# Kernel optimization log

Hardware: AMD Instinct MI355X
Metric: run time of the kernel (lower is better)

The kernel has to match this reference:

```python
import jax, jax.numpy as jnp
import numpy as np

B, T, C, UNITS = 64, 1000, 320, 320


def _lstm_scan(x_tbc, m_tb, W, U, b):
    """Masked LSTM over leading time axis.
    x_tbc: [T,B,C], m_tb: [T,B] bool. Keras gate order i,f,c(g),o.
    Masked steps carry (h,c) through unchanged and emit the carried h,
    matching Keras masking semantics. Returns (ys [T,B,U], h_T [B,U]).
    """
    units = U.shape[0]
    h0 = jnp.zeros((x_tbc.shape[1], units), x_tbc.dtype)

    def step(carry, inp):
        h, c = carry
        xt, mt = inp
        z = xt @ W + h @ U + b                      # [B, 4U]
        i, f, g, o = jnp.split(z, 4, axis=-1)
        i = jax.nn.sigmoid(i)
        f = jax.nn.sigmoid(f)
        g = jnp.tanh(g)
        o = jax.nn.sigmoid(o)
        c_new = f * c + i * g
        h_new = o * jnp.tanh(c_new)
        mt = mt[:, None]
        h = jnp.where(mt, h_new, h)
        c = jnp.where(mt, c_new, c)
        return (h, c), h

    (hT, cT), ys = jax.lax.scan(step, (h0, h0), (x_tbc, m_tb))
    return ys, hT


def setup_inputs() -> dict:
    key = jax.random.key(0)
    ks = jax.random.split(key, 8)
    inputs = jax.random.normal(ks[0], (B, T, C), dtype=jnp.float32)
    # padding mask: variable sequence lengths in [T//2, T]
    seq_len = jax.random.randint(ks[1], (B,), T // 2, T + 1)
    mask = (jnp.arange(T)[None, :] < seq_len[:, None])  # [B, T] bool
    s_in = 1.0 / np.sqrt(C)
    s_rec = 1.0 / np.sqrt(UNITS)
    W_fwd = jax.random.normal(ks[2], (C, 4 * UNITS), jnp.float32) * s_in
    U_fwd = jax.random.normal(ks[3], (UNITS, 4 * UNITS), jnp.float32) * s_rec
    b_fwd = jnp.zeros((4 * UNITS,), jnp.float32).at[UNITS:2 * UNITS].set(1.0)  # unit forget bias
    W_bwd = jax.random.normal(ks[4], (C, 4 * UNITS), jnp.float32) * s_in
    U_bwd = jax.random.normal(ks[5], (UNITS, 4 * UNITS), jnp.float32) * s_rec
    b_bwd = jnp.zeros((4 * UNITS,), jnp.float32).at[UNITS:2 * UNITS].set(1.0)
    return {"inputs": inputs, "mask": mask, "W_fwd": W_fwd, "U_fwd": U_fwd,
            "b_fwd": b_fwd, "W_bwd": W_bwd, "U_bwd": U_bwd, "b_bwd": b_bwd}


def reference(inputs, mask, W_fwd, U_fwd, b_fwd, W_bwd, U_bwd, b_bwd):
    x = jnp.transpose(inputs, (1, 0, 2))   # [T,B,C]
    m = jnp.transpose(mask, (1, 0))        # [T,B]
    # forward direction
    ys_f, h_f = _lstm_scan(x, m, W_fwd, U_fwd, b_fwd)
    # backward direction: go_backwards reverses time; Bidirectional flips output back
    ys_b, h_b = _lstm_scan(x[::-1], m[::-1], W_bwd, U_bwd, b_bwd)
    ys_b = ys_b[::-1]
    sequence_output = jnp.transpose(jnp.concatenate([ys_f, ys_b], axis=-1), (1, 0, 2))  # [B,T,2U]
    state_output = jnp.concatenate([h_f, h_b], axis=-1)  # [B,2U]
    return sequence_output, state_output
```

## Files before the change

### kernel.cpp

```cpp
#include <hip/hip_runtime.h>
#include <hip/hip_bf16.h>
#include <stdint.h>


#define Bx 64
#define Tx 1000
#define Cx 320
#define NSLICE 40
#define UPW 8

typedef __attribute__((ext_vector_type(8))) short short8;
typedef __attribute__((ext_vector_type(4))) short short4v;
typedef __attribute__((ext_vector_type(4))) float f32x4;

__device__ inline unsigned short f2bf(float f) {
  unsigned x = __builtin_bit_cast(unsigned, f);
  x += 0x7fffu + ((x >> 16) & 1u);
  return (unsigned short)(x >> 16);
}
__device__ inline float bf2f(unsigned short u) {
  unsigned x = ((unsigned)u) << 16;
  return __builtin_bit_cast(float, x);
}

#define OFF_MB   0ull
#define OFF_BAR  8192ull
#define OFF_HB   16384ull
#define OFF_XB   0ull
#define OFF_WT   40960000ull
#define OFF_BP   42598400ull
#define OFF_ZX   42608640ull

__global__ __launch_bounds__(256) void k_prep_x(const float* __restrict__ X,
                                                unsigned short* __restrict__ Xb) {
  int i4 = blockIdx.x * 256 + threadIdx.x;
  if (i4 >= Bx * Tx * Cx / 4) return;
  int idx = i4 * 4;
  int b = idx / (Tx * Cx);
  int rem = idx - b * (Tx * Cx);
  int t = rem / Cx;
  int c = rem - t * Cx;
  float4 v = *(const float4*)(X + idx);
  short4v o;
  o[0] = (short)f2bf(v.x); o[1] = (short)f2bf(v.y);
  o[2] = (short)f2bf(v.z); o[3] = (short)f2bf(v.w);
  *(short4v*)(Xb + (size_t)(t * Bx + b) * Cx + c) = o;
}

__global__ __launch_bounds__(256) void k_prep_w(const float* __restrict__ Wf,
                                                const float* __restrict__ Wb,
                                                const float* __restrict__ bfv,
                                                const float* __restrict__ bbv,
                                                unsigned short* __restrict__ Wt,
                                                float* __restrict__ biasp) {
  int gid = blockIdx.x * 256 + threadIdx.x;
  if (gid < 2 * 1280 * 320) {
    int dir = gid / (1280 * 320);
    int rem = gid - dir * 1280 * 320;
    int n = rem / 320;
    int k = rem - n * 320;
    int u = n >> 2, g = n & 3;
    const float* W = dir ? Wb : Wf;
    Wt[gid] = f2bf(W[k * 1280 + g * 320 + u]);
  }
  if (gid < 2 * 1280) {
    int dir = gid / 1280, n = gid - dir * 1280;
    int u = n >> 2, g = n & 3;
    const float* bsrc = dir ? bbv : bfv;
    biasp[gid] = bsrc[g * 320 + u];
  }
}

__global__ __launch_bounds__(256) void k_prep_mask(const void* __restrict__ maskp,
                                                   unsigned long long* __restrict__ mask2) {
  int t = blockIdx.x * 256 + threadIdx.x;
  if (t >= Tx) return;
  const unsigned* mw = (const unsigned*)maskp;
  const bool mbyte = (mw[0] == 0x01010101u);
  unsigned long long wv = 0ull;
  if (mbyte) {
    const unsigned char* m8 = (const unsigned char*)maskp;
#pragma unroll 8
    for (int b = 0; b < Bx; b++)
      wv |= (unsigned long long)(m8[b * Tx + t] & 1) << b;
  } else {
    const int* m32 = (const int*)maskp;
#pragma unroll 8
    for (int b = 0; b < Bx; b++)
      wv |= (unsigned long long)(m32[b * Tx + t] & 1) << b;
  }
  mask2[t] = wv;
}

__global__ __launch_bounds__(256) void k_gemm(const unsigned short* __restrict__ A,
                                              const unsigned short* __restrict__ Bt,
                                              const float* __restrict__ biasp,
                                              unsigned short* __restrict__ Czx) {
  int bid = blockIdx.x;
  int dir = bid / 5000;
  int r = bid - dir * 5000;
  int tm = r / 10, tn = r - (r / 10) * 10;
  long m0 = (long)tm * 128;
  int n0 = tn * 128;
  const unsigned short* Bd = Bt + (size_t)dir * 1280 * 320;
  const float* bias = biasp + dir * 1280;

  __shared__ __align__(16) unsigned short As[128 * 64];
  __shared__ __align__(16) unsigned short Bs[128 * 64];

  int tid = threadIdx.x;
  int wave = tid >> 6, lane = tid & 63;
  int l15 = lane & 15, l4 = lane >> 4;

  f32x4 acc[2][8];
#pragma unroll
  for (int i = 0; i < 2; i++)
#pragma unroll
    for (int j = 0; j < 8; j++) acc[i][j] = (f32x4){0.f, 0.f, 0.f, 0.f};

  for (int k0 = 0; k0 < 320; k0 += 64) {
    __syncthreads();
#pragma unroll
    for (int it = 0; it < 4; it++) {
      int idx = it * 256 + tid;
      int rr = idx >> 3, cc = idx & 7;
      const unsigned short* ga = A + (size_t)(m0 + rr) * 320 + k0 + cc * 8;
      unsigned short* la = As + (size_t)(it * 256 + wave * 64) * 8;
      __builtin_amdgcn_global_load_lds(
          (const __attribute__((address_space(1))) void*)ga,
          (__attribute__((address_space(3))) void*)la, 16, 0, 0);
      const unsigned short* gb = Bd + (size_t)(n0 + rr) * 320 + k0 + cc * 8;
      unsigned short* lb = Bs + (size_t)(it * 256 + wave * 64) * 8;
      __builtin_amdgcn_global_load_lds(
          (const __attribute__((address_space(1))) void*)gb,
          (__attribute__((address_space(3))) void*)lb, 16, 0, 0);
    }
    __syncthreads();
#pragma unroll
    for (int kk = 0; kk < 2; kk++) {
      short8 af[2], bf8[8];
#pragma unroll
      for (int mf = 0; mf < 2; mf++)
        af[mf] = *(const short8*)(As + (wave * 32 + mf * 16 + l15) * 64 + kk * 32 + l4 * 8);
#pragma unroll
      for (int nf = 0; nf < 8; nf++)
        bf8[nf] = *(const short8*)(Bs + (nf * 16 + l15) * 64 + kk * 32 + l4 * 8);
#pragma unroll
      for (int mf = 0; mf < 2; mf++)
#pragma unroll
        for (int nf = 0; nf < 8; nf++)
          acc[mf][nf] = __builtin_amdgcn_mfma_f32_16x16x32_bf16(af[mf], bf8[nf], acc[mf][nf], 0, 0, 0);
    }
  }
#pragma unroll
  for (int mf = 0; mf < 2; mf++) {
#pragma unroll
    for (int nf = 0; nf < 8; nf++) {
      int col = n0 + nf * 16 + l15;
      float bv = bias[col];
      int slice = col >> 5, i32v = col & 31;
      size_t sbase = ((size_t)(dir * NSLICE + slice)) * Tx * 2048;
#pragma unroll
      for (int i = 0; i < 4; i++) {
        long m = m0 + wave * 32 + mf * 16 + l4 * 4 + i;
        long t = m >> 6;
        int b = (int)(m & 63);
        Czx[sbase + (size_t)t * 2048 + b * 32 + i32v] = f2bf(acc[mf][nf][i] + bv);
      }
    }
  }
}

__global__ __launch_bounds__(256, 1) void k_lstm(const unsigned short* __restrict__ Zx,
                                                 const float* __restrict__ Uf,
                                                 const float* __restrict__ Ub,
                                                 const unsigned long long* __restrict__ mask2,
                                                 unsigned short* __restrict__ hbuf,
                                                 float* __restrict__ out,
                                                 unsigned* __restrict__ bar) {
  const int w = blockIdx.x;
  const int dir = w / NSLICE;
  const int slice = w - dir * NSLICE;
  const int u0 = slice * UPW;
  const int tid = threadIdx.x;
  const int wave = tid >> 6, lane = tid & 63;
  const int l15 = lane & 15, l4 = lane >> 4;

  const float* U = dir ? Ub : Uf;
  short8 bfrag[2][10];
#pragma unroll
  for (int nf = 0; nf < 2; nf++) {
    int i32v = nf * 16 + l15;
    int colU = (i32v & 3) * 320 + u0 + (i32v >> 2);
#pragma unroll
    for (int kt = 0; kt < 10; kt++) {
      short8 v;
#pragma unroll
      for (int j = 0; j < 8; j++)
        v[j] = (short)f2bf(U[(size_t)(kt * 32 + l4 * 8 + j) * 1280 + colU]);
      bfrag[nf][kt] = v;
    }
  }

  const int pb = tid >> 2;
  const int uu2 = (tid & 3) * 2;
  const int arow = wave * 16 + l15;
  float c0 = 0.f, c1 = 0.f, h0 = 0.f, h1 = 0.f;

  __shared__ float zsh[64][32];

  unsigned* slots = bar + (size_t)dir * NSLICE * 16;
  const unsigned short* zbase = Zx + ((size_t)(dir * NSLICE + slice)) * Tx * 2048;

  int t = dir ? (Tx - 1) : 0;
  short8 zv = *(const short8*)(zbase + (size_t)t * 2048 + tid * 8);
  unsigned long long mwrd = mask2[t];

  for (int s = 0;; ++s) {
    t = dir ? (Tx - 1 - s) : s;
    float zr[8];
    if (s > 0) {
      if (tid < NSLICE) {
        while (__hip_atomic_load(&slots[tid * 16], __ATOMIC_RELAXED,
                                 __HIP_MEMORY_SCOPE_AGENT) < (unsigned)s)
          __builtin_amdgcn_s_sleep(1);
      }
      __syncthreads();

      const unsigned short* hr = hbuf + ((size_t)((s & 1) * 2 + dir)) * Bx * 320;
      const unsigned short* hp = hr + arow * 320 + l4 * 8;
      short8 afr[10];
#pragma unroll
      for (int kt = 0; kt < 10; kt++) {
        union { unsigned long long q[2]; short8 v; } u;
        u.q[0] = __hip_atomic_load((const unsigned long long*)(hp + kt * 32),
                                   __ATOMIC_RELAXED, __HIP_MEMORY_SCOPE_AGENT);
        u.q[1] = __hip_atomic_load((const unsigned long long*)(hp + kt * 32 + 4),
                                   __ATOMIC_RELAXED, __HIP_MEMORY_SCOPE_AGENT);
        afr[kt] = u.v;
      }
#pragma unroll
      for (int nf = 0; nf < 2; nf++) {
        f32x4 a0 = {0.f, 0.f, 0.f, 0.f}, a1 = {0.f, 0.f, 0.f, 0.f};
#pragma unroll
        for (int k2 = 0; k2 < 5; k2++) {
          a0 = __builtin_amdgcn_mfma_f32_16x16x32_bf16(afr[2 * k2], bfrag[nf][2 * k2], a0, 0, 0, 0);
          a1 = __builtin_amdgcn_mfma_f32_16x16x32_bf16(afr[2 * k2 + 1], bfrag[nf][2 * k2 + 1], a1, 0, 0, 0);
        }
        int rr = wave * 16 + l4 * 4;
        zsh[rr + 0][nf * 16 + l15] = a0[0] + a1[0];
        zsh[rr + 1][nf * 16 + l15] = a0[1] + a1[1];
        zsh[rr + 2][nf * 16 + l15] = a0[2] + a1[2];
        zsh[rr + 3][nf * 16 + l15] = a0[3] + a1[3];
      }
      __syncthreads();
#pragma unroll
      for (int j = 0; j < 8; j++) zr[j] = zsh[pb][uu2 * 4 + j];
    } else {
#pragma unroll
      for (int j = 0; j < 8; j++) zr[j] = 0.f;
    }

    int mv = (int)((mwrd >> pb) & 1ull);
    {
      float zi = bf2f((unsigned short)zv[0]) + zr[0];
      float zf = bf2f((unsigned short)zv[1]) + zr[1];
      float zg = bf2f((unsigned short)zv[2]) + zr[2];
      float zo = bf2f((unsigned short)zv[3]) + zr[3];
      float ig = 1.f / (1.f + __expf(-zi));
      float fg = 1.f / (1.f + __expf(-zf));
      float gg = 2.f / (1.f + __expf(-2.f * zg)) - 1.f;
      float og = 1.f / (1.f + __expf(-zo));
      float cn = fg * c0 + ig * gg;
      float hn = og * (2.f / (1.f + __expf(-2.f * cn)) - 1.f);
      if (mv) { c0 = cn; h0 = hn; }
    }
    {
      float zi = bf2f((unsigned short)zv[4]) + zr[4];
      float zf = bf2f((unsigned short)zv[5]) + zr[5];
      float zg = bf2f((unsigned short)zv[6]) + zr[6];
      float zo = bf2f((unsigned short)zv[7]) + zr[7];
      float ig = 1.f / (1.f + __expf(-zi));
      float fg = 1.f / (1.f + __expf(-zf));
      float gg = 2.f / (1.f + __expf(-2.f * zg)) - 1.f;
      float og = 1.f / (1.f + __expf(-zo));
      float cn = fg * c1 + ig * gg;
      float hn = og * (2.f / (1.f + __expf(-2.f * cn)) - 1.f);
      if (mv) { c1 = cn; h1 = hn; }
    }

    unsigned short* hw = hbuf + ((size_t)(((s + 1) & 1) * 2 + dir)) * Bx * 320;
    unsigned hv = (unsigned)f2bf(h0) | ((unsigned)f2bf(h1) << 16);
    __hip_atomic_store((unsigned*)(hw + pb * 320 + u0 + uu2), hv,
                       __ATOMIC_RELAXED, __HIP_MEMORY_SCOPE_AGENT);

    __syncthreads();
    if (tid == 0 && s < Tx - 1)
      __hip_atomic_store(&slots[slice * 16], (unsigned)(s + 1), __ATOMIC_RELEASE,
                         __HIP_MEMORY_SCOPE_AGENT);

    *(float2*)(out + ((size_t)pb * Tx + t) * 640 + dir * 320 + u0 + uu2) =
        make_float2(h0, h1);
    if (s == Tx - 1) {
      *(float2*)(out + 40960000ull + (size_t)pb * 640 + dir * 320 + u0 + uu2) =
          make_float2(h0, h1);
      break;
    }

    int tn = dir ? (Tx - 2 - s) : (s + 1);
    zv = *(const short8*)(zbase + (size_t)tn * 2048 + tid * 8);
    mwrd = mask2[tn];
  }
}

extern "C" void kernel_launch(void* const* d_in, const int* in_sizes, int n_in,
                              void* d_out, int out_size, void* d_ws, size_t ws_size,
                              hipStream_t stream) {
  const float* X = (const float*)d_in[0];
  const void* Mk = d_in[1];
  const float* Wf = (const float*)d_in[2];
  const float* Uf = (const float*)d_in[3];
  const float* bfv = (const float*)d_in[4];
  const float* Wb = (const float*)d_in[5];
  const float* Ub = (const float*)d_in[6];
  const float* bbv = (const float*)d_in[7];

  char* ws = (char*)d_ws;
  unsigned short* Xb = (unsigned short*)(ws + OFF_XB);
  unsigned short* Wt = (unsigned short*)(ws + OFF_WT);
  float* bp = (float*)(ws + OFF_BP);
  unsigned short* Zx = (unsigned short*)(ws + OFF_ZX);
  unsigned long long* mask2 = (unsigned long long*)(ws + OFF_MB);
  unsigned short* hbuf = (unsigned short*)(ws + OFF_HB);
  unsigned* bar = (unsigned*)(ws + OFF_BAR);

  k_prep_x<<<dim3(20000), dim3(256), 0, stream>>>(X, Xb);
  k_prep_w<<<dim3(3200), dim3(256), 0, stream>>>(Wf, Wb, bfv, bbv, Wt, bp);
  k_gemm<<<dim3(10000), dim3(256), 0, stream>>>(Xb, Wt, bp, Zx);
  hipMemsetAsync(ws + OFF_BAR, 0, 5120, stream);
  k_prep_mask<<<dim3(4), dim3(256), 0, stream>>>(Mk, mask2);
  k_lstm<<<dim3(2 * NSLICE), dim3(256), 0, stream>>>(Zx, Uf, Ub, mask2, hbuf,
                                                     (float*)d_out, bar);
}
```

Baseline: 6.358 ms.

## Halve LSTM workgroups per direction, doubling units per workgroup

Changes the persistent recurrent kernel split from 40 to 20 workgroups per direction, so each handles 16 hidden units (64 gate columns), with a matching Zx layout in the GEMM epilogue. Each step now polls half as many cross-workgroup flags, which reduces grid-barrier traffic on the serial critical path. In exchange, each workgroup does twice the MFMA and gate math per step and holds twice the U fragments in registers. Output and h stores are widened to 64-bit, and the output writes switch to relaxed atomic stores.

```diff
diff --git a/kernel.cpp b/kernel.cpp
--- a/kernel.cpp
+++ b/kernel.cpp
@@ -6,8 +6,8 @@
 #define Bx 64
 #define Tx 1000
 #define Cx 320
-#define NSLICE 40
-#define UPW 8
+#define NSLICE 20
+#define UPW 16
 
 typedef __attribute__((ext_vector_type(8))) short short8;
 typedef __attribute__((ext_vector_type(4))) short short4v;
@@ -158,14 +158,14 @@
     for (int nf = 0; nf < 8; nf++) {
       int col = n0 + nf * 16 + l15;
       float bv = bias[col];
-      int slice = col >> 5, i32v = col & 31;
-      size_t sbase = ((size_t)(dir * NSLICE + slice)) * Tx * 2048;
+      int slice = col >> 6, i64v = col & 63;
+      size_t sbase = ((size_t)(dir * NSLICE + slice)) * Tx * 4096;
 #pragma unroll
       for (int i = 0; i < 4; i++) {
         long m = m0 + wave * 32 + mf * 16 + l4 * 4 + i;
         long t = m >> 6;
         int b = (int)(m & 63);
-        Czx[sbase + (size_t)t * 2048 + b * 32 + i32v] = f2bf(acc[mf][nf][i] + bv);
+        Czx[sbase + (size_t)t * 4096 + b * 64 + i64v] = f2bf(acc[mf][nf][i] + bv);
       }
     }
   }
@@ -187,11 +187,11 @@
   const int l15 = lane & 15, l4 = lane >> 4;
 
   const float* U = dir ? Ub : Uf;
-  short8 bfrag[2][10];
-#pragma unroll
-  for (int nf = 0; nf < 2; nf++) {
-    int i32v = nf * 16 + l15;
-    int colU = (i32v & 3) * 320 + u0 + (i32v >> 2);
+  short8 bfrag[4][10];
+#pragma unroll
+  for (int nf = 0; nf < 4; nf++) {
+    int ncol = nf * 16 + l15;
+    int colU = (ncol & 3) * 320 + u0 + (ncol >> 2);
 #pragma unroll
     for (int kt = 0; kt < 10; kt++) {
       short8 v;
@@ -203,22 +203,24 @@
   }
 
   const int pb = tid >> 2;
-  const int uu2 = (tid & 3) * 2;
+  const int uq = tid & 3;
   const int arow = wave * 16 + l15;
-  float c0 = 0.f, c1 = 0.f, h0 = 0.f, h1 = 0.f;
-
-  __shared__ float zsh[64][32];
-
-  unsigned* slots = bar + (size_t)dir * NSLICE * 16;
-  const unsigned short* zbase = Zx + ((size_t)(dir * NSLICE + slice)) * Tx * 2048;
+  float c0 = 0.f, c1 = 0.f, c2 = 0.f, c3 = 0.f;
+  float h0 = 0.f, h1 = 0.f, h2 = 0.f, h3 = 0.f;
+
+  __shared__ float zsh[64][68];
+
+  unsigned* slots = bar + dir * NSLICE * 16;
+  const unsigned short* zbase = Zx + ((size_t)(dir * NSLICE + slice)) * Tx * 4096;
 
   int t = dir ? (Tx - 1) : 0;
-  short8 zv = *(const short8*)(zbase + (size_t)t * 2048 + tid * 8);
+  short8 zv0 = *(const short8*)(zbase + (size_t)t * 4096 + pb * 64 + uq * 16);
+  short8 zv1 = *(const short8*)(zbase + (size_t)t * 4096 + pb * 64 + uq * 16 + 8);
   unsigned long long mwrd = mask2[t];
 
   for (int s = 0;; ++s) {
     t = dir ? (Tx - 1 - s) : s;
-    float zr[8];
+    float4 zr0, zr1, zr2, zr3;
     if (s > 0) {
       if (tid < NSLICE) {
         while (__hip_atomic_load(&slots[tid * 16], __ATOMIC_RELAXED,
@@ -240,7 +242,7 @@
         afr[kt] = u.v;
       }
 #pragma unroll
-      for (int nf = 0; nf < 2; nf++) {
+      for (int nf = 0; nf < 4; nf++) {
         f32x4 a0 = {0.f, 0.f, 0.f, 0.f}, a1 = {0.f, 0.f, 0.f, 0.f};
 #pragma unroll
         for (int k2 = 0; k2 < 5; k2++) {
@@ -254,44 +256,40 @@
         zsh[rr + 3][nf * 16 + l15] = a0[3] + a1[3];
       }
       __syncthreads();
-#pragma unroll
-      for (int j = 0; j < 8; j++) zr[j] = zsh[pb][uu2 * 4 + j];
+      zr0 = *(const float4*)&zsh[pb][uq * 16 + 0];
+      zr1 = *(const float4*)&zsh[pb][uq * 16 + 4];
+      zr2 = *(const float4*)&zsh[pb][uq * 16 + 8];
+      zr3 = *(const float4*)&zsh[pb][uq * 16 + 12];
     } else {
-#pragma unroll
-      for (int j = 0; j < 8; j++) zr[j] = 0.f;
+      zr0 = zr1 = zr2 = zr3 = make_float4(0.f, 0.f, 0.f, 0.f);
     }
 
     int mv = (int)((mwrd >> pb) & 1ull);
-    {
-      float zi = bf2f((unsigned short)zv[0]) + zr[0];
-      float zf = bf2f((unsigned short)zv[1]) + zr[1];
-      float zg = bf2f((unsigned short)zv[2]) + zr[2];
-      float zo = bf2f((unsigned short)zv[3]) + zr[3];
-      float ig = 1.f / (1.f + __expf(-zi));
-      float fg = 1.f / (1.f + __expf(-zf));
-      float gg = 2.f / (1.f + __expf(-2.f * zg)) - 1.f;
-      float og = 1.f / (1.f + __expf(-zo));
-      float cn = fg * c0 + ig * gg;
-      float hn = og * (2.f / (1.f + __expf(-2.f * cn)) - 1.f);
-      if (mv) { c0 = cn; h0 = hn; }
-    }
-    {
-      float zi = bf2f((unsigned short)zv[4]) + zr[4];
-      float zf = bf2f((unsigned short)zv[5]) + zr[5];
-      float zg = bf2f((unsigned short)zv[6]) + zr[6];
-      float zo = bf2f((unsigned short)zv[7]) + zr[7];
-      float ig = 1.f / (1.f + __expf(-zi));
-      float fg = 1.f / (1.f + __expf(-zf));
-      float gg = 2.f / (1.f + __expf(-2.f * zg)) - 1.f;
-      float og = 1.f / (1.f + __expf(-zo));
-      float cn = fg * c1 + ig * gg;
-      float hn = og * (2.f / (1.f + __expf(-2.f * cn)) - 1.f);
-      if (mv) { c1 = cn; h1 = hn; }
-    }
+#define GATES(CC, HH, Z0, Z1, Z2, Z3, ZR)                              \
+    {                                                                  \
+      float zi = bf2f((unsigned short)(Z0)) + (ZR).x;                  \
+      float zf = bf2f((unsigned short)(Z1)) + (ZR).y;                  \
+      float zg = bf2f((unsigned short)(Z2)) + (ZR).z;                  \
+      float zo = bf2f((unsigned short)(Z3)) + (ZR).w;                  \
+      float ig = 1.f / (1.f + __expf(-zi));                            \
+      float fg = 1.f / (1.f + __expf(-zf));                            \
+      float gg = 2.f / (1.f + __expf(-2.f * zg)) - 1.f;                \
+      float og = 1.f / (1.f + __expf(-zo));                            \
+      float cn = fg * (CC) + ig * gg;                                  \
+      float hn = og * (2.f / (1.f + __expf(-2.f * cn)) - 1.f);         \
+      if (mv) { (CC) = cn; (HH) = hn; }                                \
+    }
+    GATES(c0, h0, zv0[0], zv0[1], zv0[2], zv0[3], zr0)
+    GATES(c1, h1, zv0[4], zv0[5], zv0[6], zv0[7], zr1)
+    GATES(c2, h2, zv1[0], zv1[1], zv1[2], zv1[3], zr2)
+    GATES(c3, h3, zv1[4], zv1[5], zv1[6], zv1[7], zr3)
+#undef GATES
 
     unsigned short* hw = hbuf + ((size_t)(((s + 1) & 1) * 2 + dir)) * Bx * 320;
-    unsigned hv = (unsigned)f2bf(h0) | ((unsigned)f2bf(h1) << 16);
-    __hip_atomic_store((unsigned*)(hw + pb * 320 + u0 + uu2), hv,
+    unsigned long long hv =
+        (unsigned long long)f2bf(h0) | ((unsigned long long)f2bf(h1) << 16) |
+        ((unsigned long long)f2bf(h2) << 32) | ((unsigned long long)f2bf(h3) << 48);
+    __hip_atomic_store((unsigned long long*)(hw + pb * 320 + u0 + uq * 4), hv,
                        __ATOMIC_RELAXED, __HIP_MEMORY_SCOPE_AGENT);
 
     __syncthreads();
@@ -299,16 +297,23 @@
       __hip_atomic_store(&slots[slice * 16], (unsigned)(s + 1), __ATOMIC_RELEASE,
                          __HIP_MEMORY_SCOPE_AGENT);
 
-    *(float2*)(out + ((size_t)pb * Tx + t) * 640 + dir * 320 + u0 + uu2) =
-        make_float2(h0, h1);
+    union { float f[4]; unsigned long long q[2]; } ou;
+    ou.f[0] = h0; ou.f[1] = h1; ou.f[2] = h2; ou.f[3] = h3;
+    unsigned long long* op = (unsigned long long*)(out +
+        ((size_t)pb * Tx + t) * 640 + dir * 320 + u0 + uq * 4);
+    __hip_atomic_store(op, ou.q[0], __ATOMIC_RELAXED, __HIP_MEMORY_SCOPE_AGENT);
+    __hip_atomic_store(op + 1, ou.q[1], __ATOMIC_RELAXED, __HIP_MEMORY_SCOPE_AGENT);
     if (s == Tx - 1) {
-      *(float2*)(out + 40960000ull + (size_t)pb * 640 + dir * 320 + u0 + uu2) =
-          make_float2(h0, h1);
+      unsigned long long* fp = (unsigned long long*)(out + 40960000ull +
+          (size_t)pb * 640 + dir * 320 + u0 + uq * 4);
+      __hip_atomic_store(fp, ou.q[0], __ATOMIC_RELAXED, __HIP_MEMORY_SCOPE_AGENT);
+      __hip_atomic_store(fp + 1, ou.q[1], __ATOMIC_RELAXED, __HIP_MEMORY_SCOPE_AGENT);
       break;
     }
 
     int tn = dir ? (Tx - 2 - s) : (s + 1);
-    zv = *(const short8*)(zbase + (size_t)tn * 2048 + tid * 8);
+    zv0 = *(const short8*)(zbase + (size_t)tn * 4096 + pb * 64 + uq * 16);
+    zv1 = *(const short8*)(zbase + (size_t)tn * 4096 + pb * 64 + uq * 16 + 8);
     mwrd = mask2[tn];
   }
 }
@@ -337,7 +342,7 @@
   k_prep_x<<<dim3(20000), dim3(256), 0, stream>>>(X, Xb);
   k_prep_w<<<dim3(3200), dim3(256), 0, stream>>>(Wf, Wb, bfv, bbv, Wt, bp);
   k_gemm<<<dim3(10000), dim3(256), 0, stream>>>(Xb, Wt, bp, Zx);
-  hipMemsetAsync(ws + OFF_BAR, 0, 5120, stream);
+  hipMemsetAsync(ws + OFF_BAR, 0, 2560, stream);
   k_prep_mask<<<dim3(4), dim3(256), 0, stream>>>(Mk, mask2);
   k_lstm<<<dim3(2 * NSLICE), dim3(256), 0, stream>>>(Zx, Uf, Ub, mask2, hbuf,
                                                      (float*)d_out, bar);
```

Measured after the change: 5.669 ms. 10.8% less time.
